# Optimization experiments

Measured on AMD Instinct MI355X. Metric: run time of the kernel, lower is better.

The kernel has to match this reference:

```python
import jax, jax.numpy as jnp
import numpy as np

D = 768      # hidden size (hardcoded in module)
H = 8        # MHA heads
DH = D // H  # head dim = 96
SLOPE = 0.01 # LeakyReLU default negative slope
NEG = -1e9


def _leaky(x):
    return jnp.where(x >= 0, x, SLOPE * x)


def setup_inputs() -> dict:
    key = jax.random.key(0)
    ks = jax.random.split(key, 20)
    B, S, T, C, L = 32, 2048, 64, 512, 16
    seq = jax.random.normal(ks[0], (B, S, D), dtype=jnp.float32)
    tab_ids = jax.random.randint(ks[1], (B, T, L), 0, S, dtype=jnp.int32)
    col_ids = jax.random.randint(ks[2], (B, C, L), 0, S, dtype=jnp.int32)
    # contiguous column->table assignment (8 cols/table), mirrors cumulative
    # slicing by column_number_in_each_table and keeps every table non-empty
    t_of_c = jnp.broadcast_to(jnp.repeat(jnp.arange(T, dtype=jnp.int32), C // T), (B, C))
    g = lambda k, sh: (jax.random.normal(k, sh, dtype=jnp.float32) * 0.02)
    return {
        "sequence_embeddings": seq,
        "table_token_ids": tab_ids,
        "column_token_ids": col_ids,
        "table_of_column": t_of_c,
        "W_tab_pool": g(ks[3], (D, D)), "b_tab_pool": g(ks[4], (D,)),
        "W_col_pool": g(ks[5], (D, D)), "b_col_pool": g(ks[6], (D,)),
        "in_proj_w": g(ks[7], (3 * D, D)), "in_proj_b": g(ks[8], (3 * D,)),
        "out_proj_w": g(ks[9], (D, D)), "out_proj_b": g(ks[10], (D,)),
        "W_t1": g(ks[11], (D, 256)), "b_t1": g(ks[12], (256,)),
        "W_t2": g(ks[13], (256, 2)), "b_t2": g(ks[14], (2,)),
        "W_c1": g(ks[15], (D, 256)), "b_c1": g(ks[16], (256,)),
        "W_c2": g(ks[17], (256, 2)), "b_c2": g(ks[18], (2,)),
    }


def reference(sequence_embeddings, table_token_ids, column_token_ids, table_of_column,
              W_tab_pool, b_tab_pool, W_col_pool, b_col_pool,
              in_proj_w, in_proj_b, out_proj_w, out_proj_b,
              W_t1, b_t1, W_t2, b_t2, W_c1, b_c1, W_c2, b_c2):
    B, T = table_token_ids.shape[:2]
    C = column_token_ids.shape[1]
    bi = jnp.arange(B)[:, None, None]
    # ragged span sum-pooling (gather + segment sum)
    tab = sequence_embeddings[bi, table_token_ids].sum(axis=2)   # [B,T,D]
    col = sequence_embeddings[bi, column_token_ids].sum(axis=2)  # [B,C,D]
    tab = _leaky(tab @ W_tab_pool + b_tab_pool)
    col = _leaky(col @ W_col_pool + b_col_pool)
    # per-table cross-attention (table query over its own columns), batched + masked
    Wq, Wk, Wv = jnp.split(in_proj_w, 3, axis=0)
    bq, bk, bv = jnp.split(in_proj_b, 3, axis=0)
    q = (tab @ Wq.T + bq).reshape(B, T, H, DH)
    k = (col @ Wk.T + bk).reshape(B, C, H, DH)
    v = (col @ Wv.T + bv).reshape(B, C, H, DH)
    scores = jnp.einsum('bthd,bchd->bhtc', q, k) / jnp.sqrt(jnp.float32(DH))
    mask = table_of_column[:, None, None, :] == jnp.arange(T, dtype=table_of_column.dtype)[None, None, :, None]
    attn = jax.nn.softmax(jnp.where(mask, scores, NEG), axis=-1)
    ctx = jnp.einsum('bhtc,bchd->bthd', attn, v).reshape(B, T, D)
    tab = tab + (ctx @ out_proj_w.T + out_proj_b)
    tab = tab / jnp.maximum(jnp.linalg.norm(tab, axis=-1, keepdims=True), 1e-12)
    # classification heads (dropout in eval mode = identity)
    t_logits = _leaky(tab @ W_t1 + b_t1) @ W_t2 + b_t2  # [B,T,2]
    c_logits = _leaky(col @ W_c1 + b_c1) @ W_c2 + b_c2  # [B,C,2]
    return jnp.concatenate([t_logits, c_logits], axis=1)  # [B,T+C,2]
```

## Files before the change

### kernel.cpp

```cpp
#include <hip/hip_runtime.h>
#include <hip/hip_bf16.h>

constexpr int Bc = 32;
constexpr int Sc = 2048;
constexpr int Tc = 64;
constexpr int Cc = 512;
constexpr int Lc = 16;
constexpr int Dc = 768;
constexpr int Hc = 8;
constexpr int DHc = 96;

typedef __attribute__((ext_vector_type(4))) float f32x4;
typedef __attribute__((ext_vector_type(8))) short bf16x8;
typedef __hip_bfloat16 bf;

__device__ inline unsigned short f2bf(float f) {
  __hip_bfloat16 h = __float2bfloat16(f);
  return *reinterpret_cast<unsigned short*>(&h);
}
__device__ inline float us2f(unsigned short u) {
  return __uint_as_float(((unsigned)u) << 16);
}

#define GLDS16(gp, lp)                                                        \
  __builtin_amdgcn_global_load_lds(                                           \
      (const __attribute__((address_space(1))) void*)(gp),                    \
      (__attribute__((address_space(3))) void*)(lp), 16, 0, 0)

__device__ inline void transpose32(const float* __restrict__ in,
                                   bf* __restrict__ outp, int K, int N,
                                   int ti, float (*t)[33]) {
  int nx = N >> 5;
  int bx = (ti % nx) * 32, by = (ti / nx) * 32;
  int x = threadIdx.x & 31, y = threadIdx.x >> 5;
#pragma unroll
  for (int i = 0; i < 32; i += 8)
    t[y + i][x] = in[(size_t)(by + y + i) * N + bx + x];
  __syncthreads();
#pragma unroll
  for (int i = 0; i < 32; i += 8)
    outp[(size_t)(bx + y + i) * K + by + x] = __float2bfloat16(t[x][y + i]);
}

__global__ __launch_bounds__(256) void prep_kernel(
    const float* __restrict__ W_tab_pool, const float* __restrict__ W_col_pool,
    const float* __restrict__ W_t1, const float* __restrict__ W_c1,
    const float* __restrict__ in_proj_w, const float* __restrict__ out_proj_w,
    const float* __restrict__ b_t2, const float* __restrict__ b_c2,
    const float* __restrict__ seq, const int* __restrict__ t_of_c,
    bf* __restrict__ wtab_t, bf* __restrict__ wcol_t, bf* __restrict__ wt1_t,
    bf* __restrict__ wc1_t, bf* __restrict__ winproj, bf* __restrict__ woutproj,
    float* __restrict__ outd, ushort* __restrict__ seqb,
    int* __restrict__ col_sorted, int* __restrict__ offs,
    float* __restrict__ ssq) {
  __shared__ float t[32][33];
  __shared__ int cnt[Tc];
  __shared__ int cur[Tc + 1];
  int blk = blockIdx.x, tid = threadIdx.x;
  if (blk < 576) {
    transpose32(W_tab_pool, wtab_t, Dc, Dc, blk, t);
  } else if (blk < 1152) {
    transpose32(W_col_pool, wcol_t, Dc, Dc, blk - 576, t);
  } else if (blk < 1344) {
    transpose32(W_t1, wt1_t, Dc, 256, blk - 1152, t);
  } else if (blk < 1536) {
    transpose32(W_c1, wc1_t, Dc, 256, blk - 1344, t);
  } else if (blk < 3264) {
    int i = (blk - 1536) * 256 + tid;
    float4 v = reinterpret_cast<const float4*>(in_proj_w)[i];
    reinterpret_cast<ushort4*>(winproj)[i] =
        make_ushort4(f2bf(v.x), f2bf(v.y), f2bf(v.z), f2bf(v.w));
  } else if (blk < 3840) {
    int i = (blk - 3264) * 256 + tid;
    float4 v = reinterpret_cast<const float4*>(out_proj_w)[i];
    reinterpret_cast<ushort4*>(woutproj)[i] =
        make_ushort4(f2bf(v.x), f2bf(v.y), f2bf(v.z), f2bf(v.w));
  } else if (blk < 3984) {
    int e = (blk - 3840) * 256 + tid;
    int i = e & 1;
    int r = (e >> 1) % (Tc + Cc);
    outd[e] = (r < Tc) ? b_t2[i] : b_c2[i];
  } else if (blk < 28560) {
    int i0 = (blk - 3984) * 512 + tid;
    const float4* s4 = reinterpret_cast<const float4*>(seq);
    ushort4* o4 = reinterpret_cast<ushort4*>(seqb);
    float4 v = s4[i0];
    o4[i0] = make_ushort4(f2bf(v.x), f2bf(v.y), f2bf(v.z), f2bf(v.w));
    float4 v2 = s4[i0 + 256];
    o4[i0 + 256] = make_ushort4(f2bf(v2.x), f2bf(v2.y), f2bf(v2.z), f2bf(v2.w));
  } else if (blk < 28592) {
    int b = blk - 28560;
    if (tid < Tc) cnt[tid] = 0;
    __syncthreads();
    for (int c = tid; c < Cc; c += 256) atomicAdd(&cnt[t_of_c[b * Cc + c]], 1);
    __syncthreads();
    if (tid == 0) {
      int off = 0;
      for (int tt = 0; tt < Tc; ++tt) {
        cur[tt] = off;
        off += cnt[tt];
      }
      cur[Tc] = off;
    }
    __syncthreads();
    if (tid <= Tc) offs[b * (Tc + 1) + tid] = cur[tid];
    __syncthreads();
    for (int c = tid; c < Cc; c += 256) {
      int tt = t_of_c[b * Cc + c];
      int pos = atomicAdd(&cur[tt], 1);
      col_sorted[b * Cc + pos] = c;
    }
  } else {
#pragma unroll
    for (int i = 0; i < 8; ++i) ssq[tid * 8 + i] = 0.f;
  }
}

__global__ __launch_bounds__(256) void pool_kernel(
    const ushort* __restrict__ seqb, const int* __restrict__ tab_ids,
    const int* __restrict__ col_ids, ushort* __restrict__ tabp,
    ushort* __restrict__ colp) {
  int swz = (blockIdx.x & 7) * 576 + (blockIdx.x >> 3);
  int w = threadIdx.x >> 6, l = threadIdx.x & 63;
  int row = swz * 4 + w;
  int b = row / (Tc + Cc), r = row % (Tc + Cc);
  const int* ids;
  ushort* outp;
  if (r < Tc) {
    ids = tab_ids + ((size_t)b * Tc + r) * Lc;
    outp = tabp + ((size_t)b * Tc + r) * Dc;
  } else {
    int c = r - Tc;
    ids = col_ids + ((size_t)b * Cc + c) * Lc;
    outp = colp + ((size_t)b * Cc + c) * Dc;
  }
  float a0[4] = {0, 0, 0, 0}, a1[4] = {0, 0, 0, 0}, a2[4] = {0, 0, 0, 0};
#pragma unroll
  for (int tix = 0; tix < Lc; ++tix) {
    const ushort4* p =
        reinterpret_cast<const ushort4*>(seqb + ((size_t)b * Sc + ids[tix]) * Dc);
    ushort4 u0 = p[l], u1 = p[l + 64], u2 = p[l + 128];
    a0[0] += us2f(u0.x); a0[1] += us2f(u0.y); a0[2] += us2f(u0.z); a0[3] += us2f(u0.w);
    a1[0] += us2f(u1.x); a1[1] += us2f(u1.y); a1[2] += us2f(u1.z); a1[3] += us2f(u1.w);
    a2[0] += us2f(u2.x); a2[1] += us2f(u2.y); a2[2] += us2f(u2.z); a2[3] += us2f(u2.w);
  }
  ushort4* ob = reinterpret_cast<ushort4*>(outp);
  ob[l] = make_ushort4(f2bf(a0[0]), f2bf(a0[1]), f2bf(a0[2]), f2bf(a0[3]));
  ob[l + 64] = make_ushort4(f2bf(a1[0]), f2bf(a1[1]), f2bf(a1[2]), f2bf(a1[3]));
  ob[l + 128] = make_ushort4(f2bf(a2[0]), f2bf(a2[1]), f2bf(a2[2]), f2bf(a2[3]));
}

__device__ __forceinline__ void gemm_core(
    const bf* __restrict__ A, const bf* __restrict__ Bt,
    const float* __restrict__ bias, bf* __restrict__ Obf,
    float* __restrict__ Of32, const float* __restrict__ w2,
    float* __restrict__ outd, int out_base, int log2rpb,
    const float* __restrict__ tabf, float* __restrict__ ssq,
    const float* __restrict__ ssrd, int bx, int by, int N, int leaky,
    int outmode) {
  constexpr int BM = 128, BN = 128, BK = 64, K = Dc;
  __shared__ bf As[2][BM * BK];
  __shared__ bf Bs[2][BN * BK];
  int tid = threadIdx.x;
  int row0 = by * BM, col0 = bx * BN;
  int w = tid >> 6, l = tid & 63;
  int wr = (w >> 1) * 64, wc = (w & 1) * 64;
  f32x4 acc[4][4];
#pragma unroll
  for (int m = 0; m < 4; ++m)
#pragma unroll
    for (int n = 0; n < 4; ++n) acc[m][n] = f32x4{0.f, 0.f, 0.f, 0.f};

  int srow = tid >> 3, skk = (tid & 7) * 8;
  const bf* gA = A + (size_t)(row0 + srow) * K + skk;
  const bf* gB = Bt + (size_t)(col0 + srow) * K + skk;
  char* lA = (char*)&As[0][0] + tid * 16;
  char* lB = (char*)&Bs[0][0] + tid * 16;
  int lr = l & 15, lk = (l >> 4) * 8;

#pragma unroll
  for (int c = 0; c < 4; ++c) {
    GLDS16(gA + (size_t)c * 32 * K, lA + c * 4096);
    GLDS16(gB + (size_t)c * 32 * K, lB + c * 4096);
  }
  __syncthreads();
  int cur = 0;
  for (int k0 = 0; k0 < K; k0 += BK) {
    if (k0 + BK < K) {
      int nb = cur ^ 1;
#pragma unroll
      for (int c = 0; c < 4; ++c) {
        GLDS16(gA + k0 + BK + (size_t)c * 32 * K, lA + nb * 16384 + c * 4096);
        GLDS16(gB + k0 + BK + (size_t)c * 32 * K, lB + nb * 16384 + c * 4096);
      }
    }
    bf16x8 af[2][4], bfr[2][4];
#pragma unroll
    for (int ks = 0; ks < 2; ++ks) {
#pragma unroll
      for (int m = 0; m < 4; ++m)
        af[ks][m] = *reinterpret_cast<const bf16x8*>(
            &As[cur][(wr + m * 16 + lr) * BK + ks * 32 + lk]);
#pragma unroll
      for (int n = 0; n < 4; ++n)
        bfr[ks][n] = *reinterpret_cast<const bf16x8*>(
            &Bs[cur][(wc + n * 16 + lr) * BK + ks * 32 + lk]);
    }
#pragma unroll
    for (int ks = 0; ks < 2; ++ks)
#pragma unroll
      for (int m = 0; m < 4; ++m)
#pragma unroll
        for (int n = 0; n < 4; ++n)
          acc[m][n] = __builtin_amdgcn_mfma_f32_16x16x32_bf16(
              af[ks][m], bfr[ks][n], acc[m][n], 0, 0, 0);
    if (k0 + BK < K) __syncthreads();
    cur ^= 1;
  }

  int colI = l & 15, rowb = (l >> 4) * 4;
  if (outmode == 3) {
    float w20[4], w21[4], bv[4];
#pragma unroll
    for (int n = 0; n < 4; ++n) {
      int c = col0 + wc + n * 16 + colI;
      w20[n] = w2[c * 2];
      w21[n] = w2[c * 2 + 1];
      bv[n] = bias[c];
    }
    float scr[4][4];
#pragma unroll
    for (int m = 0; m < 4; ++m)
#pragma unroll
      for (int j = 0; j < 4; ++j) {
        if (ssrd) {
          int r = row0 + wr + m * 16 + rowb + j;
          scr[m][j] = 1.f / fmaxf(sqrtf(ssrd[r]), 1e-12f);
        } else {
          scr[m][j] = 1.f;
        }
      }
    float p0[4][4], p1[4][4];
#pragma unroll
    for (int m = 0; m < 4; ++m)
#pragma unroll
      for (int j = 0; j < 4; ++j) { p0[m][j] = 0.f; p1[m][j] = 0.f; }
#pragma unroll
    for (int m = 0; m < 4; ++m)
#pragma unroll
      for (int n = 0; n < 4; ++n)
#pragma unroll
        for (int j = 0; j < 4; ++j) {
          float v = scr[m][j] * acc[m][n][j] + bv[n];
          v = v >= 0.f ? v : 0.01f * v;
          p0[m][j] += v * w20[n];
          p1[m][j] += v * w21[n];
        }
#pragma unroll
    for (int m = 0; m < 4; ++m)
#pragma unroll
      for (int j = 0; j < 4; ++j) {
#pragma unroll
        for (int msk = 1; msk <= 8; msk <<= 1) {
          p0[m][j] += __shfl_xor(p0[m][j], msk);
          p1[m][j] += __shfl_xor(p1[m][j], msk);
        }
      }
    if (colI == 0) {
#pragma unroll
      for (int m = 0; m < 4; ++m)
#pragma unroll
        for (int j = 0; j < 4; ++j) {
          int grow = row0 + wr + m * 16 + rowb + j;
          int bb = grow >> log2rpb;
          int rr = grow & ((1 << log2rpb) - 1);
          int orow = bb * (Tc + Cc) + out_base + rr;
          atomicAdd(&outd[(size_t)orow * 2], p0[m][j]);
          atomicAdd(&outd[(size_t)orow * 2 + 1], p1[m][j]);
        }
    }
    return;
  }
  if (outmode == 4) {
    float sq[4][4];
#pragma unroll
    for (int m = 0; m < 4; ++m)
#pragma unroll
      for (int j = 0; j < 4; ++j) sq[m][j] = 0.f;
#pragma unroll
    for (int m = 0; m < 4; ++m)
#pragma unroll
      for (int n = 0; n < 4; ++n) {
        int c = col0 + wc + n * 16 + colI;
        float bv = bias[c];
#pragma unroll
        for (int j = 0; j < 4; ++j) {
          int r = row0 + wr + m * 16 + rowb + j;
          float x = acc[m][n][j] + bv + tabf[(size_t)r * N + c];
          Obf[(size_t)r * N + c] = __float2bfloat16(x);
          sq[m][j] += x * x;
        }
      }
#pragma unroll
    for (int m = 0; m < 4; ++m)
#pragma unroll
      for (int j = 0; j < 4; ++j) {
#pragma unroll
        for (int msk = 1; msk <= 8; msk <<= 1)
          sq[m][j] += __shfl_xor(sq[m][j], msk);
      }
    if (colI == 0) {
#pragma unroll
      for (int m = 0; m < 4; ++m)
#pragma unroll
        for (int j = 0; j < 4; ++j)
          atomicAdd(&ssq[row0 + wr + m * 16 + rowb + j], sq[m][j]);
    }
    return;
  }
#pragma unroll
  for (int m = 0; m < 4; ++m) {
#pragma unroll
    for (int n = 0; n < 4; ++n) {
      int c = col0 + wc + n * 16 + colI;
      float bv = bias ? bias[c] : 0.f;
#pragma unroll
      for (int j = 0; j < 4; ++j) {
        int r = row0 + wr + m * 16 + rowb + j;
        float v = acc[m][n][j] + bv;
        if (leaky) v = v >= 0.f ? v : 0.01f * v;
        Obf[(size_t)r * N + c] = __float2bfloat16(v);
        if (outmode == 2 && Of32) Of32[(size_t)r * N + c] = v;
      }
    }
  }
}

__global__ __launch_bounds__(256) void gemm_pools(
    const bf* __restrict__ tabp, const bf* __restrict__ colp,
    const bf* __restrict__ wtab_t, const bf* __restrict__ wcol_t,
    const float* __restrict__ b_tab, const float* __restrict__ b_col,
    bf* __restrict__ tabb_bf, float* __restrict__ tabb_f,
    bf* __restrict__ colb) {
  int id = (blockIdx.x & 7) * 108 + (blockIdx.x >> 3);
  const bf* Aa; const bf* Bb; const float* bb; bf* Oo; float* Ff;
  int bx, by;
  if (id < 96) {
    Aa = tabp; Bb = wtab_t; bb = b_tab; Oo = tabb_bf; Ff = tabb_f;
    bx = id % 6; by = id / 6;
  } else {
    int r = id - 96;
    Aa = colp; Bb = wcol_t; bb = b_col; Oo = colb; Ff = nullptr;
    bx = r % 6; by = r / 6;
  }
  gemm_core(Aa, Bb, bb, Oo, Ff, nullptr, nullptr, 0, 0, nullptr, nullptr,
            nullptr, bx, by, Dc, 1, 2);
}

__global__ __launch_bounds__(256) void gemm_qkv(
    const bf* __restrict__ tabb_bf, const bf* __restrict__ colb,
    const bf* __restrict__ winproj, const float* __restrict__ in_proj_b,
    bf* __restrict__ qb, bf* __restrict__ kvb) {
  int id = (blockIdx.x & 7) * 204 + (blockIdx.x >> 3);
  const bf* Aa; const bf* Bb; const float* bb; bf* Oo;
  int bx, by, NN;
  if (id < 96) {
    Aa = tabb_bf; Bb = winproj; bb = in_proj_b; Oo = qb;
    bx = id % 6; by = id / 6; NN = Dc;
  } else {
    int r = id - 96;
    Aa = colb; Bb = winproj + (size_t)Dc * Dc; bb = in_proj_b + Dc; Oo = kvb;
    bx = r % 12; by = r / 12; NN = 1536;
  }
  gemm_core(Aa, Bb, bb, Oo, nullptr, nullptr, nullptr, 0, 0, nullptr, nullptr,
            nullptr, bx, by, NN, 0, 0);
}

__global__ __launch_bounds__(256) void gemm_oc(
    const bf* __restrict__ ctxb, const bf* __restrict__ woutproj,
    const float* __restrict__ out_proj_b, const float* __restrict__ tabb_f,
    bf* __restrict__ xbf, float* __restrict__ ssq, const bf* __restrict__ colb,
    const bf* __restrict__ wc1_t, const float* __restrict__ b_c1,
    const float* __restrict__ W_c2, float* __restrict__ outd) {
  int id = (blockIdx.x & 7) * 44 + (blockIdx.x >> 3);
  if (id < 96) {
    gemm_core(ctxb, woutproj, out_proj_b, xbf, nullptr, nullptr, nullptr, 0, 0,
              tabb_f, ssq, nullptr, id % 6, id / 6, Dc, 0, 4);
  } else {
    int r = id - 96;
    gemm_core(colb, wc1_t, b_c1, nullptr, nullptr, W_c2, outd, Tc, 9, nullptr,
              nullptr, nullptr, r % 2, r / 2, 256, 1, 3);
  }
}

__global__ __launch_bounds__(256) void gemm_t1(
    const bf* __restrict__ xbf, const bf* __restrict__ wt1_t,
    const float* __restrict__ b_t1, const float* __restrict__ W_t2,
    const float* __restrict__ ssq, float* __restrict__ outd) {
  int id = (blockIdx.x & 7) * 4 + (blockIdx.x >> 3);
  gemm_core(xbf, wt1_t, b_t1, nullptr, nullptr, W_t2, outd, 0, 6, nullptr,
            nullptr, ssq, id % 2, id / 2, 256, 1, 3);
}

__global__ __launch_bounds__(256) void attn_kernel(
    const bf* __restrict__ q, const bf* __restrict__ kv,
    const int* __restrict__ col_sorted, const int* __restrict__ offs,
    bf* __restrict__ ctx) {
  int b = blockIdx.x / Tc;
  int t = blockIdx.x % Tc;
  __shared__ float pbuf[Hc][Cc];
  __shared__ float den[Hc];
  __shared__ int cols_s[Cc];
  int tid = threadIdx.x;
  int o0 = offs[b * (Tc + 1) + t];
  int n = offs[b * (Tc + 1) + t + 1] - o0;
  for (int i = tid; i < n; i += 256)
    cols_s[i] = col_sorted[(size_t)b * Cc + o0 + i];
  __syncthreads();
  int h = tid >> 5, l32 = tid & 31, g = l32 >> 3, i8 = l32 & 7;
  const float scale = 0.10206207261596577f;
  float q12[12];
  {
    const ushort* qp =
        (const ushort*)q + ((size_t)b * Tc + t) * Dc + h * DHc + i8 * 12;
    ushort4 u0 = *(const ushort4*)(qp);
    ushort4 u1 = *(const ushort4*)(qp + 4);
    ushort4 u2 = *(const ushort4*)(qp + 8);
    q12[0] = us2f(u0.x); q12[1] = us2f(u0.y); q12[2] = us2f(u0.z); q12[3] = us2f(u0.w);
    q12[4] = us2f(u1.x); q12[5] = us2f(u1.y); q12[6] = us2f(u1.z); q12[7] = us2f(u1.w);
    q12[8] = us2f(u2.x); q12[9] = us2f(u2.y); q12[10] = us2f(u2.z); q12[11] = us2f(u2.w);
  }
  if (n > 0) {
    for (int jb = 0; jb < n; jb += 4) {
      int j = jb + g;
      float s = 0.f;
      if (j < n) {
        const ushort* kp = (const ushort*)kv +
                           ((size_t)b * Cc + cols_s[j]) * 1536 + h * DHc + i8 * 12;
        ushort4 u0 = *(const ushort4*)(kp);
        ushort4 u1 = *(const ushort4*)(kp + 4);
        ushort4 u2 = *(const ushort4*)(kp + 8);
        s += q12[0] * us2f(u0.x) + q12[1] * us2f(u0.y) + q12[2] * us2f(u0.z) +
             q12[3] * us2f(u0.w);
        s += q12[4] * us2f(u1.x) + q12[5] * us2f(u1.y) + q12[6] * us2f(u1.z) +
             q12[7] * us2f(u1.w);
        s += q12[8] * us2f(u2.x) + q12[9] * us2f(u2.y) + q12[10] * us2f(u2.z) +
             q12[11] * us2f(u2.w);
      }
      s += __shfl_xor(s, 1);
      s += __shfl_xor(s, 2);
      s += __shfl_xor(s, 4);
      if (j < n && i8 == 0) pbuf[h][j] = s * scale;
    }
  }
  __syncthreads();
  if (n > 0) {
    float lmax = -3.0e38f;
    for (int j = l32; j < n; j += 32) lmax = fmaxf(lmax, pbuf[h][j]);
#pragma unroll
    for (int m = 16; m >= 1; m >>= 1) lmax = fmaxf(lmax, __shfl_xor(lmax, m));
    float lsum = 0.f;
    for (int j = l32; j < n; j += 32) {
      float e = __expf(pbuf[h][j] - lmax);
      pbuf[h][j] = e;
      lsum += e;
    }
#pragma unroll
    for (int m = 16; m >= 1; m >>= 1) lsum += __shfl_xor(lsum, m);
    if (l32 == 0) den[h] = lsum;
  } else if (l32 == 0) {
    den[h] = (float)Cc;
  }
  __syncthreads();
  int ncols = n > 0 ? n : Cc;
  float a12[12];
#pragma unroll
  for (int d = 0; d < 12; ++d) a12[d] = 0.f;
  for (int jb = 0; jb < ncols; jb += 4) {
    int j = jb + g;
    if (j < ncols) {
      int cj = n > 0 ? cols_s[j] : j;
      float pw = n > 0 ? pbuf[h][j] : 1.f;
      const ushort* vp = (const ushort*)kv + ((size_t)b * Cc + cj) * 1536 +
                         768 + h * DHc + i8 * 12;
      ushort4 u0 = *(const ushort4*)(vp);
      ushort4 u1 = *(const ushort4*)(vp + 4);
      ushort4 u2 = *(const ushort4*)(vp + 8);
      a12[0] += pw * us2f(u0.x); a12[1] += pw * us2f(u0.y);
      a12[2] += pw * us2f(u0.z); a12[3] += pw * us2f(u0.w);
      a12[4] += pw * us2f(u1.x); a12[5] += pw * us2f(u1.y);
      a12[6] += pw * us2f(u1.z); a12[7] += pw * us2f(u1.w);
      a12[8] += pw * us2f(u2.x); a12[9] += pw * us2f(u2.y);
      a12[10] += pw * us2f(u2.z); a12[11] += pw * us2f(u2.w);
    }
  }
#pragma unroll
  for (int d = 0; d < 12; ++d) {
    a12[d] += __shfl_xor(a12[d], 8);
    a12[d] += __shfl_xor(a12[d], 16);
  }
  float inv = 1.0f / den[h];
  if (g == 0) {
    ushort* cp = (ushort*)ctx + ((size_t)b * Tc + t) * Dc + h * DHc + i8 * 12;
    *(ushort4*)(cp) = make_ushort4(f2bf(a12[0] * inv), f2bf(a12[1] * inv),
                                   f2bf(a12[2] * inv), f2bf(a12[3] * inv));
    *(ushort4*)(cp + 4) = make_ushort4(f2bf(a12[4] * inv), f2bf(a12[5] * inv),
                                       f2bf(a12[6] * inv), f2bf(a12[7] * inv));
    *(ushort4*)(cp + 8) = make_ushort4(f2bf(a12[8] * inv), f2bf(a12[9] * inv),
                                       f2bf(a12[10] * inv), f2bf(a12[11] * inv));
  }
}

extern "C" void kernel_launch(void* const* d_in, const int* in_sizes, int n_in,
                              void* d_out, int out_size, void* d_ws,
                              size_t ws_size, hipStream_t stream) {
  const float* seq = (const float*)d_in[0];
  const int* tab_ids = (const int*)d_in[1];
  const int* col_ids = (const int*)d_in[2];
  const int* t_of_c = (const int*)d_in[3];
  const float* W_tab_pool = (const float*)d_in[4];
  const float* b_tab_pool = (const float*)d_in[5];
  const float* W_col_pool = (const float*)d_in[6];
  const float* b_col_pool = (const float*)d_in[7];
  const float* in_proj_w = (const float*)d_in[8];
  const float* in_proj_b = (const float*)d_in[9];
  const float* out_proj_w = (const float*)d_in[10];
  const float* out_proj_b = (const float*)d_in[11];
  const float* W_t1 = (const float*)d_in[12];
  const float* b_t1 = (const float*)d_in[13];
  const float* W_t2 = (const float*)d_in[14];
  const float* b_t2 = (const float*)d_in[15];
  const float* W_c1 = (const float*)d_in[16];
  const float* b_c1 = (const float*)d_in[17];
  const float* W_c2 = (const float*)d_in[18];
  const float* b_c2 = (const float*)d_in[19];
  float* out = (float*)d_out;

  char* p = (char*)d_ws;
  auto alloc = [&](size_t bytes) -> char* {
    char* r = p;
    p += (bytes + 255) & ~(size_t)255;
    return r;
  };
  const size_t nBT = (size_t)Bc * Tc;
  const size_t nBC = (size_t)Bc * Cc;
  ushort* seqb = (ushort*)alloc((size_t)Bc * Sc * Dc * 2);
  bf* tabp = (bf*)alloc(nBT * Dc * 2);
  bf* colp = (bf*)alloc(nBC * Dc * 2);
  bf* tabb_bf = (bf*)alloc(nBT * Dc * 2);
  float* tabb_f = (float*)alloc(nBT * Dc * 4);
  bf* colb = (bf*)alloc(nBC * Dc * 2);
  bf* qb = (bf*)alloc(nBT * Dc * 2);
  bf* kvb = (bf*)alloc(nBC * 1536 * 2);
  bf* ctxb = (bf*)alloc(nBT * Dc * 2);
  bf* xbf = (bf*)alloc(nBT * Dc * 2);
  float* ssq = (float*)alloc(nBT * 4);
  bf* wtab_t = (bf*)alloc((size_t)Dc * Dc * 2);
  bf* wcol_t = (bf*)alloc((size_t)Dc * Dc * 2);
  bf* winproj = (bf*)alloc((size_t)3 * Dc * Dc * 2);
  bf* woutproj = (bf*)alloc((size_t)Dc * Dc * 2);
  bf* wt1_t = (bf*)alloc((size_t)256 * Dc * 2);
  bf* wc1_t = (bf*)alloc((size_t)256 * Dc * 2);
  int* col_sorted = (int*)alloc(nBC * 4);
  int* offs = (int*)alloc((size_t)Bc * (Tc + 1) * 4);

  prep_kernel<<<28593, 256, 0, stream>>>(
      W_tab_pool, W_col_pool, W_t1, W_c1, in_proj_w, out_proj_w, b_t2, b_c2,
      seq, t_of_c, wtab_t, wcol_t, wt1_t, wc1_t, winproj, woutproj, out, seqb,
      col_sorted, offs, ssq);
  pool_kernel<<<Bc * (Tc + Cc) / 4, 256, 0, stream>>>(seqb, tab_ids, col_ids,
                                                      (ushort*)tabp,
                                                      (ushort*)colp);
  gemm_pools<<<864, 256, 0, stream>>>(tabp, colp, wtab_t, wcol_t, b_tab_pool,
                                      b_col_pool, tabb_bf, tabb_f, colb);
  gemm_qkv<<<1632, 256, 0, stream>>>(tabb_bf, colb, winproj, in_proj_b, qb,
                                     kvb);
  attn_kernel<<<Bc * Tc, 256, 0, stream>>>(qb, kvb, col_sorted, offs, ctxb);
  gemm_oc<<<352, 256, 0, stream>>>(ctxb, woutproj, out_proj_b, tabb_f, xbf,
                                   ssq, colb, wc1_t, b_c1, W_c2, out);
  gemm_t1<<<32, 256, 0, stream>>>(xbf, wt1_t, b_t1, W_t2, ssq, out);
}
```

Measured before the change: 577.3 us.

## Pool directly from fp32 sequence, single-buffer GEMM, fuse c1 head into attention

Removes the full bf16 conversion pass over the sequence tensor. The pooling kernel now gathers the fp32 rows directly, so it no longer writes a ~100MB bf16 copy and reads it back. The GEMM core drops LDS double-buffering in favour of a single buffer with two barriers per k-step, and adds an occupancy hint of 4 blocks per CU. The column classification head GEMM moves from the out-projection launch into the attention launch, so it overlaps with attention, and out-proj becomes its own small kernel. The trade-off is that gathers now read twice the bytes per row and the GEMM loses load/compute overlap.

```diff
diff --git a/kernel.cpp b/kernel.cpp
--- a/kernel.cpp
+++ b/kernel.cpp
@@ -47,12 +47,11 @@
     const float* __restrict__ W_t1, const float* __restrict__ W_c1,
     const float* __restrict__ in_proj_w, const float* __restrict__ out_proj_w,
     const float* __restrict__ b_t2, const float* __restrict__ b_c2,
-    const float* __restrict__ seq, const int* __restrict__ t_of_c,
-    bf* __restrict__ wtab_t, bf* __restrict__ wcol_t, bf* __restrict__ wt1_t,
-    bf* __restrict__ wc1_t, bf* __restrict__ winproj, bf* __restrict__ woutproj,
-    float* __restrict__ outd, ushort* __restrict__ seqb,
-    int* __restrict__ col_sorted, int* __restrict__ offs,
-    float* __restrict__ ssq) {
+    const int* __restrict__ t_of_c, bf* __restrict__ wtab_t,
+    bf* __restrict__ wcol_t, bf* __restrict__ wt1_t, bf* __restrict__ wc1_t,
+    bf* __restrict__ winproj, bf* __restrict__ woutproj,
+    float* __restrict__ outd, int* __restrict__ col_sorted,
+    int* __restrict__ offs, float* __restrict__ ssq) {
   __shared__ float t[32][33];
   __shared__ int cnt[Tc];
   __shared__ int cur[Tc + 1];
@@ -80,16 +79,8 @@
     int i = e & 1;
     int r = (e >> 1) % (Tc + Cc);
     outd[e] = (r < Tc) ? b_t2[i] : b_c2[i];
-  } else if (blk < 28560) {
-    int i0 = (blk - 3984) * 512 + tid;
-    const float4* s4 = reinterpret_cast<const float4*>(seq);
-    ushort4* o4 = reinterpret_cast<ushort4*>(seqb);
-    float4 v = s4[i0];
-    o4[i0] = make_ushort4(f2bf(v.x), f2bf(v.y), f2bf(v.z), f2bf(v.w));
-    float4 v2 = s4[i0 + 256];
-    o4[i0 + 256] = make_ushort4(f2bf(v2.x), f2bf(v2.y), f2bf(v2.z), f2bf(v2.w));
-  } else if (blk < 28592) {
-    int b = blk - 28560;
+  } else if (blk < 4016) {
+    int b = blk - 3984;
     if (tid < Tc) cnt[tid] = 0;
     __syncthreads();
     for (int c = tid; c < Cc; c += 256) atomicAdd(&cnt[t_of_c[b * Cc + c]], 1);
@@ -117,7 +108,7 @@
 }
 
 __global__ __launch_bounds__(256) void pool_kernel(
-    const ushort* __restrict__ seqb, const int* __restrict__ tab_ids,
+    const float* __restrict__ seq, const int* __restrict__ tab_ids,
     const int* __restrict__ col_ids, ushort* __restrict__ tabp,
     ushort* __restrict__ colp) {
   int swz = (blockIdx.x & 7) * 576 + (blockIdx.x >> 3);
@@ -134,20 +125,20 @@
     ids = col_ids + ((size_t)b * Cc + c) * Lc;
     outp = colp + ((size_t)b * Cc + c) * Dc;
   }
-  float a0[4] = {0, 0, 0, 0}, a1[4] = {0, 0, 0, 0}, a2[4] = {0, 0, 0, 0};
+  float4 a0 = {0, 0, 0, 0}, a1 = {0, 0, 0, 0}, a2 = {0, 0, 0, 0};
 #pragma unroll
   for (int tix = 0; tix < Lc; ++tix) {
-    const ushort4* p =
-        reinterpret_cast<const ushort4*>(seqb + ((size_t)b * Sc + ids[tix]) * Dc);
-    ushort4 u0 = p[l], u1 = p[l + 64], u2 = p[l + 128];
-    a0[0] += us2f(u0.x); a0[1] += us2f(u0.y); a0[2] += us2f(u0.z); a0[3] += us2f(u0.w);
-    a1[0] += us2f(u1.x); a1[1] += us2f(u1.y); a1[2] += us2f(u1.z); a1[3] += us2f(u1.w);
-    a2[0] += us2f(u2.x); a2[1] += us2f(u2.y); a2[2] += us2f(u2.z); a2[3] += us2f(u2.w);
+    const float4* p =
+        reinterpret_cast<const float4*>(seq + ((size_t)b * Sc + ids[tix]) * Dc);
+    float4 v0 = p[l], v1 = p[l + 64], v2 = p[l + 128];
+    a0.x += v0.x; a0.y += v0.y; a0.z += v0.z; a0.w += v0.w;
+    a1.x += v1.x; a1.y += v1.y; a1.z += v1.z; a1.w += v1.w;
+    a2.x += v2.x; a2.y += v2.y; a2.z += v2.z; a2.w += v2.w;
   }
   ushort4* ob = reinterpret_cast<ushort4*>(outp);
-  ob[l] = make_ushort4(f2bf(a0[0]), f2bf(a0[1]), f2bf(a0[2]), f2bf(a0[3]));
-  ob[l + 64] = make_ushort4(f2bf(a1[0]), f2bf(a1[1]), f2bf(a1[2]), f2bf(a1[3]));
-  ob[l + 128] = make_ushort4(f2bf(a2[0]), f2bf(a2[1]), f2bf(a2[2]), f2bf(a2[3]));
+  ob[l] = make_ushort4(f2bf(a0.x), f2bf(a0.y), f2bf(a0.z), f2bf(a0.w));
+  ob[l + 64] = make_ushort4(f2bf(a1.x), f2bf(a1.y), f2bf(a1.z), f2bf(a1.w));
+  ob[l + 128] = make_ushort4(f2bf(a2.x), f2bf(a2.y), f2bf(a2.z), f2bf(a2.w));
 }
 
 __device__ __forceinline__ void gemm_core(
@@ -159,8 +150,8 @@
     const float* __restrict__ ssrd, int bx, int by, int N, int leaky,
     int outmode) {
   constexpr int BM = 128, BN = 128, BK = 64, K = Dc;
-  __shared__ bf As[2][BM * BK];
-  __shared__ bf Bs[2][BN * BK];
+  __shared__ bf As[BM * BK];
+  __shared__ bf Bs[BN * BK];
   int tid = threadIdx.x;
   int row0 = by * BM, col0 = bx * BN;
   int w = tid >> 6, l = tid & 63;
@@ -174,48 +165,36 @@
   int srow = tid >> 3, skk = (tid & 7) * 8;
   const bf* gA = A + (size_t)(row0 + srow) * K + skk;
   const bf* gB = Bt + (size_t)(col0 + srow) * K + skk;
-  char* lA = (char*)&As[0][0] + tid * 16;
-  char* lB = (char*)&Bs[0][0] + tid * 16;
+  char* lA = (char*)As + tid * 16;
+  char* lB = (char*)Bs + tid * 16;
   int lr = l & 15, lk = (l >> 4) * 8;
 
-#pragma unroll
-  for (int c = 0; c < 4; ++c) {
-    GLDS16(gA + (size_t)c * 32 * K, lA + c * 4096);
-    GLDS16(gB + (size_t)c * 32 * K, lB + c * 4096);
-  }
-  __syncthreads();
-  int cur = 0;
   for (int k0 = 0; k0 < K; k0 += BK) {
-    if (k0 + BK < K) {
-      int nb = cur ^ 1;
-#pragma unroll
-      for (int c = 0; c < 4; ++c) {
-        GLDS16(gA + k0 + BK + (size_t)c * 32 * K, lA + nb * 16384 + c * 4096);
-        GLDS16(gB + k0 + BK + (size_t)c * 32 * K, lB + nb * 16384 + c * 4096);
-      }
-    }
-    bf16x8 af[2][4], bfr[2][4];
+#pragma unroll
+    for (int c = 0; c < 4; ++c) {
+      GLDS16(gA + k0 + (size_t)c * 32 * K, lA + c * 4096);
+      GLDS16(gB + k0 + (size_t)c * 32 * K, lB + c * 4096);
+    }
+    __syncthreads();
 #pragma unroll
     for (int ks = 0; ks < 2; ++ks) {
+      bf16x8 af[4], bfr[4];
 #pragma unroll
       for (int m = 0; m < 4; ++m)
-        af[ks][m] = *reinterpret_cast<const bf16x8*>(
-            &As[cur][(wr + m * 16 + lr) * BK + ks * 32 + lk]);
+        af[m] = *reinterpret_cast<const bf16x8*>(
+            &As[(wr + m * 16 + lr) * BK + ks * 32 + lk]);
 #pragma unroll
       for (int n = 0; n < 4; ++n)
-        bfr[ks][n] = *reinterpret_cast<const bf16x8*>(
-            &Bs[cur][(wc + n * 16 + lr) * BK + ks * 32 + lk]);
-    }
-#pragma unroll
-    for (int ks = 0; ks < 2; ++ks)
+        bfr[n] = *reinterpret_cast<const bf16x8*>(
+            &Bs[(wc + n * 16 + lr) * BK + ks * 32 + lk]);
 #pragma unroll
       for (int m = 0; m < 4; ++m)
 #pragma unroll
         for (int n = 0; n < 4; ++n)
           acc[m][n] = __builtin_amdgcn_mfma_f32_16x16x32_bf16(
-              af[ks][m], bfr[ks][n], acc[m][n], 0, 0, 0);
-    if (k0 + BK < K) __syncthreads();
-    cur ^= 1;
+              af[m], bfr[n], acc[m][n], 0, 0, 0);
+    }
+    __syncthreads();
   }
 
   int colI = l & 15, rowb = (l >> 4) * 4;
@@ -336,64 +315,49 @@
   }
 }
 
-__global__ __launch_bounds__(256) void gemm_pools(
+__global__ __launch_bounds__(256, 4) void gemm_pools(
     const bf* __restrict__ tabp, const bf* __restrict__ colp,
     const bf* __restrict__ wtab_t, const bf* __restrict__ wcol_t,
     const float* __restrict__ b_tab, const float* __restrict__ b_col,
     bf* __restrict__ tabb_bf, float* __restrict__ tabb_f,
     bf* __restrict__ colb) {
   int id = (blockIdx.x & 7) * 108 + (blockIdx.x >> 3);
-  const bf* Aa; const bf* Bb; const float* bb; bf* Oo; float* Ff;
-  int bx, by;
   if (id < 96) {
-    Aa = tabp; Bb = wtab_t; bb = b_tab; Oo = tabb_bf; Ff = tabb_f;
-    bx = id % 6; by = id / 6;
+    gemm_core(tabp, wtab_t, b_tab, tabb_bf, tabb_f, nullptr, nullptr, 0, 0,
+              nullptr, nullptr, nullptr, id % 6, id / 6, Dc, 1, 2);
   } else {
     int r = id - 96;
-    Aa = colp; Bb = wcol_t; bb = b_col; Oo = colb; Ff = nullptr;
-    bx = r % 6; by = r / 6;
-  }
-  gemm_core(Aa, Bb, bb, Oo, Ff, nullptr, nullptr, 0, 0, nullptr, nullptr,
-            nullptr, bx, by, Dc, 1, 2);
-}
-
-__global__ __launch_bounds__(256) void gemm_qkv(
+    gemm_core(colp, wcol_t, b_col, colb, nullptr, nullptr, nullptr, 0, 0,
+              nullptr, nullptr, nullptr, r % 6, r / 6, Dc, 1, 0);
+  }
+}
+
+__global__ __launch_bounds__(256, 4) void gemm_qkv(
     const bf* __restrict__ tabb_bf, const bf* __restrict__ colb,
     const bf* __restrict__ winproj, const float* __restrict__ in_proj_b,
     bf* __restrict__ qb, bf* __restrict__ kvb) {
   int id = (blockIdx.x & 7) * 204 + (blockIdx.x >> 3);
-  const bf* Aa; const bf* Bb; const float* bb; bf* Oo;
-  int bx, by, NN;
   if (id < 96) {
-    Aa = tabb_bf; Bb = winproj; bb = in_proj_b; Oo = qb;
-    bx = id % 6; by = id / 6; NN = Dc;
+    gemm_core(tabb_bf, winproj, in_proj_b, qb, nullptr, nullptr, nullptr, 0, 0,
+              nullptr, nullptr, nullptr, id % 6, id / 6, Dc, 0, 0);
   } else {
     int r = id - 96;
-    Aa = colb; Bb = winproj + (size_t)Dc * Dc; bb = in_proj_b + Dc; Oo = kvb;
-    bx = r % 12; by = r / 12; NN = 1536;
-  }
-  gemm_core(Aa, Bb, bb, Oo, nullptr, nullptr, nullptr, 0, 0, nullptr, nullptr,
-            nullptr, bx, by, NN, 0, 0);
-}
-
-__global__ __launch_bounds__(256) void gemm_oc(
+    gemm_core(colb, winproj + (size_t)Dc * Dc, in_proj_b + Dc, kvb, nullptr,
+              nullptr, nullptr, 0, 0, nullptr, nullptr, nullptr, r % 12,
+              r / 12, 1536, 0, 0);
+  }
+}
+
+__global__ __launch_bounds__(256, 4) void gemm_outproj(
     const bf* __restrict__ ctxb, const bf* __restrict__ woutproj,
     const float* __restrict__ out_proj_b, const float* __restrict__ tabb_f,
-    bf* __restrict__ xbf, float* __restrict__ ssq, const bf* __restrict__ colb,
-    const bf* __restrict__ wc1_t, const float* __restrict__ b_c1,
-    const float* __restrict__ W_c2, float* __restrict__ outd) {
-  int id = (blockIdx.x & 7) * 44 + (blockIdx.x >> 3);
-  if (id < 96) {
-    gemm_core(ctxb, woutproj, out_proj_b, xbf, nullptr, nullptr, nullptr, 0, 0,
-              tabb_f, ssq, nullptr, id % 6, id / 6, Dc, 0, 4);
-  } else {
-    int r = id - 96;
-    gemm_core(colb, wc1_t, b_c1, nullptr, nullptr, W_c2, outd, Tc, 9, nullptr,
-              nullptr, nullptr, r % 2, r / 2, 256, 1, 3);
-  }
-}
-
-__global__ __launch_bounds__(256) void gemm_t1(
+    bf* __restrict__ xbf, float* __restrict__ ssq) {
+  int id = (blockIdx.x & 7) * 12 + (blockIdx.x >> 3);
+  gemm_core(ctxb, woutproj, out_proj_b, xbf, nullptr, nullptr, nullptr, 0, 0,
+            tabb_f, ssq, nullptr, id % 6, id / 6, Dc, 0, 4);
+}
+
+__global__ __launch_bounds__(256, 4) void gemm_t1(
     const bf* __restrict__ xbf, const bf* __restrict__ wt1_t,
     const float* __restrict__ b_t1, const float* __restrict__ W_t2,
     const float* __restrict__ ssq, float* __restrict__ outd) {
@@ -402,12 +366,21 @@
             nullptr, ssq, id % 2, id / 2, 256, 1, 3);
 }
 
-__global__ __launch_bounds__(256) void attn_kernel(
+__global__ __launch_bounds__(256) void attn_c1_kernel(
     const bf* __restrict__ q, const bf* __restrict__ kv,
     const int* __restrict__ col_sorted, const int* __restrict__ offs,
-    bf* __restrict__ ctx) {
-  int b = blockIdx.x / Tc;
-  int t = blockIdx.x % Tc;
+    bf* __restrict__ ctx, const bf* __restrict__ colb,
+    const bf* __restrict__ wc1_t, const float* __restrict__ b_c1,
+    const float* __restrict__ W_c2, float* __restrict__ outd) {
+  int id = (blockIdx.x & 7) * 288 + (blockIdx.x >> 3);
+  if (id >= 2048) {
+    int r = id - 2048;
+    gemm_core(colb, wc1_t, b_c1, nullptr, nullptr, W_c2, outd, Tc, 9, nullptr,
+              nullptr, nullptr, r % 2, r / 2, 256, 1, 3);
+    return;
+  }
+  int b = id / Tc;
+  int t = id % Tc;
   __shared__ float pbuf[Hc][Cc];
   __shared__ float den[Hc];
   __shared__ int cols_s[Cc];
@@ -544,7 +517,6 @@
   };
   const size_t nBT = (size_t)Bc * Tc;
   const size_t nBC = (size_t)Bc * Cc;
-  ushort* seqb = (ushort*)alloc((size_t)Bc * Sc * Dc * 2);
   bf* tabp = (bf*)alloc(nBT * Dc * 2);
   bf* colp = (bf*)alloc(nBC * Dc * 2);
   bf* tabb_bf = (bf*)alloc(nBT * Dc * 2);
@@ -564,19 +536,21 @@
   int* col_sorted = (int*)alloc(nBC * 4);
   int* offs = (int*)alloc((size_t)Bc * (Tc + 1) * 4);
 
-  prep_kernel<<<28593, 256, 0, stream>>>(
-      W_tab_pool, W_col_pool, W_t1, W_c1, in_proj_w, out_proj_w, b_t2, b_c2,
-      seq, t_of_c, wtab_t, wcol_t, wt1_t, wc1_t, winproj, woutproj, out, seqb,
-      col_sorted, offs, ssq);
-  pool_kernel<<<Bc * (Tc + Cc) / 4, 256, 0, stream>>>(seqb, tab_ids, col_ids,
+  prep_kernel<<<4017, 256, 0, stream>>>(W_tab_pool, W_col_pool, W_t1, W_c1,
+                                        in_proj_w, out_proj_w, b_t2, b_c2,
+                                        t_of_c, wtab_t, wcol_t, wt1_t, wc1_t,
+                                        winproj, woutproj, out, col_sorted,
+                                        offs, ssq);
+  pool_kernel<<<Bc * (Tc + Cc) / 4, 256, 0, stream>>>(seq, tab_ids, col_ids,
                                                       (ushort*)tabp,
                                                       (ushort*)colp);
   gemm_pools<<<864, 256, 0, stream>>>(tabp, colp, wtab_t, wcol_t, b_tab_pool,
                                       b_col_pool, tabb_bf, tabb_f, colb);
   gemm_qkv<<<1632, 256, 0, stream>>>(tabb_bf, colb, winproj, in_proj_b, qb,
                                      kvb);
-  attn_kernel<<<Bc * Tc, 256, 0, stream>>>(qb, kvb, col_sorted, offs, ctxb);
-  gemm_oc<<<352, 256, 0, stream>>>(ctxb, woutproj, out_proj_b, tabb_f, xbf,
-                                   ssq, colb, wc1_t, b_c1, W_c2, out);
+  attn_c1_kernel<<<2304, 256, 0, stream>>>(qb, kvb, col_sorted, offs, ctxb,
+                                           colb, wc1_t, b_c1, W_c2, out);
+  gemm_outproj<<<96, 256, 0, stream>>>(ctxb, woutproj, out_proj_b, tabb_f, xbf,
+                                       ssq);
   gemm_t1<<<32, 256, 0, stream>>>(xbf, wt1_t, b_t1, W_t2, ssq, out);
 }
```

After: 586.1 us. About the same (+1.5%).
